# Kernel tuning notes

Measured on AMD Instinct MI355X. Metric: run time of the kernel, lower is better.

The kernel has to match this reference:

```python
import jax, jax.numpy as jnp
import numpy as np

N_NODES = 100000
N_EDGES = 800000
D = 128


def setup_inputs() -> dict:
    key = jax.random.key(0)
    ks = jax.random.split(key, 6)
    x = jax.random.normal(ks[0], (N_NODES, D), dtype=jnp.float32)
    src = jax.random.randint(ks[1], (N_EDGES,), 0, N_NODES, dtype=jnp.int64 if jax.config.jax_enable_x64 else jnp.int32)
    dst = jax.random.randint(ks[2], (N_EDGES,), 0, N_NODES, dtype=jnp.int64 if jax.config.jax_enable_x64 else jnp.int32)
    W_self = jax.random.normal(ks[3], (D, D), dtype=jnp.float32) / np.sqrt(D)
    W_neigh = jax.random.normal(ks[4], (D, D), dtype=jnp.float32) / np.sqrt(D)
    b = jax.random.normal(ks[5], (D,), dtype=jnp.float32) * 0.01
    return {"x": x, "src": src, "dst": dst, "W_self": W_self, "W_neigh": W_neigh, "b": b}


def reference(x, src, dst, W_self, W_neigh, b):
    # DGL SAGEConv('mean'): mean-aggregate source features over incoming edges.
    msgs = x[src]  # [E, D] gather (irregular)
    sums = jax.ops.segment_sum(msgs, dst, num_segments=N_NODES)  # [N, D]
    deg = jax.ops.segment_sum(jnp.ones((msgs.shape[0],), dtype=x.dtype), dst,
                              num_segments=N_NODES)
    # DGL clamps in-degree to at least 1 (zero-in-degree nodes get zero h_neigh).
    h_neigh = sums / jnp.maximum(deg, 1.0)[:, None]
    # rst = fc_self(h) + fc_neigh(h_neigh) + bias, then ReLU activation.
    out = x @ W_self + h_neigh @ W_neigh + b
    return jax.nn.relu(out)
```

## Files before the change

kernel.cpp:

```cpp
#include <hip/hip_runtime.h>
#include <stdint.h>

#define N_NODES 100000
#define N_EDGES 800000
#define D 128

typedef _Float16 f16x8 __attribute__((ext_vector_type(8)));
typedef float f32x4 __attribute__((ext_vector_type(4)));


__global__ void hist_rank(const int* __restrict__ dst, int* __restrict__ cnt,
                          int* __restrict__ rank) {
    int e = blockIdx.x * blockDim.x + threadIdx.x;
    if (e < N_EDGES) rank[e] = atomicAdd(&cnt[dst[e]], 1);
}

__global__ void scan_local(const int* __restrict__ cnt, int* __restrict__ offsets,
                           int* __restrict__ bs) {
    __shared__ int sdata[256];
    const int t = threadIdx.x;
    const int base = blockIdx.x * 1024 + t * 4;
    int v[4];
    int s = 0;
#pragma unroll
    for (int j = 0; j < 4; ++j) {
        int i = base + j;
        v[j] = (i < N_NODES) ? cnt[i] : 0;
        s += v[j];
    }
    sdata[t] = s;
    __syncthreads();
    int incl = s;
    for (int off = 1; off < 256; off <<= 1) {
        int add = (t >= off) ? sdata[t - off] : 0;
        __syncthreads();
        incl += add;
        sdata[t] = incl;
        __syncthreads();
    }
    int run = incl - s;
#pragma unroll
    for (int j = 0; j < 4; ++j) {
        int i = base + j;
        if (i < N_NODES) offsets[i] = run;
        run += v[j];
    }
    if (t == 255) bs[blockIdx.x] = incl;
}

__global__ void scan_block2(int* __restrict__ bs, int* __restrict__ offsets, int nblk) {
    int t = threadIdx.x;
    int v0 = (2 * t < nblk) ? bs[2 * t] : 0;
    int v1 = (2 * t + 1 < nblk) ? bs[2 * t + 1] : 0;
    int s = v0 + v1;
    int incl = s;
    for (int off = 1; off < 64; off <<= 1) {
        int n = __shfl_up(incl, off, 64);
        if (t >= off) incl += n;
    }
    int excl = incl - s;
    if (2 * t < nblk) bs[2 * t] = excl;
    if (2 * t + 1 < nblk) bs[2 * t + 1] = excl + v0;
    if (t == 63) offsets[N_NODES] = incl;
}

__global__ void scan_add(int* __restrict__ offsets, const int* __restrict__ bs) {
    const int t = threadIdx.x;
    const int base = blockIdx.x * 1024 + t * 4;
    const int add = bs[blockIdx.x];
#pragma unroll
    for (int j = 0; j < 4; ++j) {
        int i = base + j;
        if (i < N_NODES) offsets[i] += add;
    }
}

__global__ void scatter2(const int* __restrict__ src, const int* __restrict__ dst,
                         const int* __restrict__ offsets, const int* __restrict__ rank,
                         int* __restrict__ esrc) {
    int e = blockIdx.x * blockDim.x + threadIdx.x;
    if (e < N_EDGES) esrc[offsets[dst[e]] + rank[e]] = src[e];
}

__global__ __launch_bounds__(256) void gemm_reg(const float* __restrict__ x,
                                                const float* __restrict__ Ws,
                                                const float* __restrict__ Wn,
                                                const float* __restrict__ bias,
                                                float* __restrict__ pre,
                                                _Float16* __restrict__ y2) {
    const int half = blockIdx.x & 1;
    const int bid = blockIdx.x >> 1;
    const int nb = gridDim.x >> 1;
    const int tid = threadIdx.x;
    const int w = tid >> 6;
    const int lane = tid & 63;
    const int lr = lane & 15;
    const int lk = (lane >> 4) * 8;
    const int wc = w & 1;
    const int ws_ = w >> 1;

    const float* __restrict__ W = half ? Wn : Ws;

    f16x8 bfrag[4][4];
#pragma unroll
    for (int ks = 0; ks < 4; ++ks) {
#pragma unroll
        for (int fc = 0; fc < 4; ++fc) {
            const int col = wc * 64 + fc * 16 + lr;
            const int kb = ks * 32 + lk;
            f16x8 h;
#pragma unroll
            for (int j = 0; j < 8; ++j) h[j] = (_Float16)W[(long)(kb + j) * D + col];
            bfrag[ks][fc] = h;
        }
    }
    float bv[4];
    if (half == 0) {
#pragma unroll
        for (int fc = 0; fc < 4; ++fc) bv[fc] = bias[wc * 64 + fc * 16 + lr];
    }

    auto loadA = [&](f32x4* A, int s) {
        const float* __restrict__ xr = &x[(long)(s * 16 + lr) * D];
#pragma unroll
        for (int ks = 0; ks < 4; ++ks) {
            A[2 * ks] = *(const f32x4*)&xr[ks * 32 + lk];
            A[2 * ks + 1] = *(const f32x4*)&xr[ks * 32 + lk + 4];
        }
    };
    auto compStore = [&](const f32x4* A, int s) {
        f32x4 acc[4];
#pragma unroll
        for (int fc = 0; fc < 4; ++fc) acc[fc] = (f32x4){0.f, 0.f, 0.f, 0.f};
#pragma unroll
        for (int ks = 0; ks < 4; ++ks) {
            f16x8 af;
#pragma unroll
            for (int j = 0; j < 4; ++j) {
                af[j] = (_Float16)A[2 * ks][j];
                af[4 + j] = (_Float16)A[2 * ks + 1][j];
            }
#pragma unroll
            for (int fc = 0; fc < 4; ++fc)
                acc[fc] = __builtin_amdgcn_mfma_f32_16x16x32_f16(af, bfrag[ks][fc],
                                                                 acc[fc], 0, 0, 0);
        }
        const int rb = s * 16 + (lane >> 4) * 4;
        if (half == 0) {
#pragma unroll
            for (int fc = 0; fc < 4; ++fc) {
                const int col = wc * 64 + fc * 16 + lr;
#pragma unroll
                for (int i = 0; i < 4; ++i)
                    pre[(long)(rb + i) * D + col] = acc[fc][i] + bv[fc];
            }
        } else {
#pragma unroll
            for (int fc = 0; fc < 4; ++fc) {
                const int col = wc * 64 + fc * 16 + lr;
#pragma unroll
                for (int i = 0; i < 4; ++i)
                    y2[(long)(rb + i) * D + col] = (_Float16)acc[fc][i];
            }
        }
    };

    const int nstrip = N_NODES / 16;
    const int stride = nb * 2;
    int s = bid * 2 + ws_;
    int snext = s + stride;

    f32x4 A0[8], A1[8];
    loadA(A0, s);
    while (true) {
        bool hn = snext < nstrip;
        if (hn) loadA(A1, snext);
        compStore(A0, s);
        if (!hn) break;
        s = snext;
        snext += stride;
        hn = snext < nstrip;
        if (hn) loadA(A0, snext);
        compStore(A1, s);
        if (!hn) break;
        s = snext;
        snext += stride;
    }
}

__global__ __launch_bounds__(256) void agg_wave(const _Float16* __restrict__ y2,
                                                const int* __restrict__ offsets,
                                                const int* __restrict__ esrc,
                                                float* __restrict__ out) {
    const int n = blockIdx.x * 4 + (threadIdx.x >> 6);
    const int lane = threadIdx.x & 63;
    const int slot = lane >> 4;
    const int c8 = lane & 15;
    const int s = offsets[n];
    const int e = offsets[n + 1];
    float a[8] = {0.f, 0.f, 0.f, 0.f, 0.f, 0.f, 0.f, 0.f};
    for (int j = s + slot; j < e; j += 4) {
        int sn = esrc[j];
        f16x8 v = *(const f16x8*)&y2[(long)sn * D + c8 * 8];
#pragma unroll
        for (int i = 0; i < 8; ++i) a[i] += (float)v[i];
    }
#pragma unroll
    for (int i = 0; i < 8; ++i) {
        a[i] += __shfl_xor(a[i], 16, 64);
        a[i] += __shfl_xor(a[i], 32, 64);
    }
    if (slot == 0) {
        const int deg = e - s;
        const float inv = (deg > 0) ? 1.f / (float)deg : 0.f;
        float4 p0 = *(const float4*)&out[(long)n * D + c8 * 8];
        float4 p1 = *(const float4*)&out[(long)n * D + c8 * 8 + 4];
        float4 o0, o1;
        o0.x = fmaxf(p0.x + a[0] * inv, 0.f);
        o0.y = fmaxf(p0.y + a[1] * inv, 0.f);
        o0.z = fmaxf(p0.z + a[2] * inv, 0.f);
        o0.w = fmaxf(p0.w + a[3] * inv, 0.f);
        o1.x = fmaxf(p1.x + a[4] * inv, 0.f);
        o1.y = fmaxf(p1.y + a[5] * inv, 0.f);
        o1.z = fmaxf(p1.z + a[6] * inv, 0.f);
        o1.w = fmaxf(p1.w + a[7] * inv, 0.f);
        *(float4*)&out[(long)n * D + c8 * 8] = o0;
        *(float4*)&out[(long)n * D + c8 * 8 + 4] = o1;
    }
}


extern "C" void kernel_launch(void* const* d_in, const int* in_sizes, int n_in,
                              void* d_out, int out_size, void* d_ws, size_t ws_size,
                              hipStream_t stream) {
    const float* x  = (const float*)d_in[0];
    const int* src  = (const int*)d_in[1];
    const int* dst  = (const int*)d_in[2];
    const float* Ws = (const float*)d_in[3];
    const float* Wn = (const float*)d_in[4];
    const float* b  = (const float*)d_in[5];
    float* out = (float*)d_out;

    int* cnt     = (int*)d_ws;
    int* offsets = cnt + N_NODES;
    int* bs      = offsets + N_NODES + 1;
    int* rank    = bs + 128;
    int* esrc    = rank + N_EDGES;
    uintptr_t p = (uintptr_t)(esrc + N_EDGES);
    p = (p + 255) & ~(uintptr_t)255;
    _Float16* y2 = (_Float16*)p;

    const int nblk_scan = (N_NODES + 1023) / 1024;

    hipMemsetAsync(cnt, 0, N_NODES * sizeof(int), stream);
    hist_rank<<<(N_EDGES + 255) / 256, 256, 0, stream>>>(dst, cnt, rank);
    scan_local<<<nblk_scan, 256, 0, stream>>>(cnt, offsets, bs);
    scan_block2<<<1, 64, 0, stream>>>(bs, offsets, nblk_scan);
    scan_add<<<nblk_scan, 256, 0, stream>>>(offsets, bs);
    scatter2<<<(N_EDGES + 255) / 256, 256, 0, stream>>>(src, dst, offsets, rank, esrc);
    gemm_reg<<<1024, 256, 0, stream>>>(x, Ws, Wn, b, out, y2);
    agg_wave<<<N_NODES / 4, 256, 0, stream>>>(y2, offsets, esrc, out);
}
```

Measured before the change: 241.8 us.

## Fuse CSR build into one cooperative kernel with grid syncs

Replaces the memset plus five separate CSR-construction kernels (histogram, three scan stages, scatter) with a single cooperative kernel that uses grid-wide syncs between phases. This removes several kernel launch boundaries and their idle gaps. It also changes the gemm grid from 1024 to 1280 blocks. The risk is that each grid.sync costs time of its own, and the fixed 512-block grid may use the GPU less fully in the edge-parallel phases.

```diff
diff --git a/kernel.cpp b/kernel.cpp
--- a/kernel.cpp
+++ b/kernel.cpp
@@ -1,85 +1,102 @@
 #include <hip/hip_runtime.h>
+#include <hip/hip_cooperative_groups.h>
 #include <stdint.h>
+
+namespace cg = cooperative_groups;
 
 #define N_NODES 100000
 #define N_EDGES 800000
 #define D 128
+#define CSR_BLOCKS 512
+#define CSR_THREADS 256
 
 typedef _Float16 f16x8 __attribute__((ext_vector_type(8)));
 typedef float f32x4 __attribute__((ext_vector_type(4)));
 
-
-__global__ void hist_rank(const int* __restrict__ dst, int* __restrict__ cnt,
-                          int* __restrict__ rank) {
-    int e = blockIdx.x * blockDim.x + threadIdx.x;
-    if (e < N_EDGES) rank[e] = atomicAdd(&cnt[dst[e]], 1);
-}
-
-__global__ void scan_local(const int* __restrict__ cnt, int* __restrict__ offsets,
-                           int* __restrict__ bs) {
-    __shared__ int sdata[256];
+__global__ __launch_bounds__(CSR_THREADS) void csr_coop(const int* __restrict__ src,
+                                                        const int* __restrict__ dst,
+                                                        int* __restrict__ cnt,
+                                                        int* __restrict__ offsets,
+                                                        int* __restrict__ bs,
+                                                        int* __restrict__ rank,
+                                                        int* __restrict__ esrc) {
+    cg::grid_group grid = cg::this_grid();
+    __shared__ int sdata[CSR_THREADS];
     const int t = threadIdx.x;
-    const int base = blockIdx.x * 1024 + t * 4;
+    const int bid = blockIdx.x;
+    const int gtid = bid * CSR_THREADS + t;
+    const int gstride = CSR_BLOCKS * CSR_THREADS;
+
+    for (int i = gtid; i < N_NODES; i += gstride) cnt[i] = 0;
+    grid.sync();
+
+    for (int e = gtid; e < N_EDGES; e += gstride)
+        rank[e] = atomicAdd(&cnt[dst[e]], 1);
+    grid.sync();
+
+    const int nblk = (N_NODES + 1023) / 1024;
     int v[4];
-    int s = 0;
-#pragma unroll
-    for (int j = 0; j < 4; ++j) {
-        int i = base + j;
-        v[j] = (i < N_NODES) ? cnt[i] : 0;
-        s += v[j];
-    }
-    sdata[t] = s;
-    __syncthreads();
-    int incl = s;
-    for (int off = 1; off < 256; off <<= 1) {
-        int add = (t >= off) ? sdata[t - off] : 0;
+    int run_keep = 0;
+    if (bid < nblk) {
+        const int base = bid * 1024 + t * 4;
+        int s = 0;
+#pragma unroll
+        for (int j = 0; j < 4; ++j) {
+            int i = base + j;
+            v[j] = (i < N_NODES) ? cnt[i] : 0;
+            s += v[j];
+        }
+        sdata[t] = s;
         __syncthreads();
-        incl += add;
-        sdata[t] = incl;
-        __syncthreads();
-    }
-    int run = incl - s;
-#pragma unroll
-    for (int j = 0; j < 4; ++j) {
-        int i = base + j;
-        if (i < N_NODES) offsets[i] = run;
-        run += v[j];
-    }
-    if (t == 255) bs[blockIdx.x] = incl;
-}
-
-__global__ void scan_block2(int* __restrict__ bs, int* __restrict__ offsets, int nblk) {
-    int t = threadIdx.x;
-    int v0 = (2 * t < nblk) ? bs[2 * t] : 0;
-    int v1 = (2 * t + 1 < nblk) ? bs[2 * t + 1] : 0;
-    int s = v0 + v1;
-    int incl = s;
-    for (int off = 1; off < 64; off <<= 1) {
-        int n = __shfl_up(incl, off, 64);
-        if (t >= off) incl += n;
-    }
-    int excl = incl - s;
-    if (2 * t < nblk) bs[2 * t] = excl;
-    if (2 * t + 1 < nblk) bs[2 * t + 1] = excl + v0;
-    if (t == 63) offsets[N_NODES] = incl;
-}
-
-__global__ void scan_add(int* __restrict__ offsets, const int* __restrict__ bs) {
-    const int t = threadIdx.x;
-    const int base = blockIdx.x * 1024 + t * 4;
-    const int add = bs[blockIdx.x];
-#pragma unroll
-    for (int j = 0; j < 4; ++j) {
-        int i = base + j;
-        if (i < N_NODES) offsets[i] += add;
-    }
-}
-
-__global__ void scatter2(const int* __restrict__ src, const int* __restrict__ dst,
-                         const int* __restrict__ offsets, const int* __restrict__ rank,
-                         int* __restrict__ esrc) {
-    int e = blockIdx.x * blockDim.x + threadIdx.x;
-    if (e < N_EDGES) esrc[offsets[dst[e]] + rank[e]] = src[e];
+        int incl = s;
+        for (int off = 1; off < CSR_THREADS; off <<= 1) {
+            int add = (t >= off) ? sdata[t - off] : 0;
+            __syncthreads();
+            incl += add;
+            sdata[t] = incl;
+            __syncthreads();
+        }
+        int run = incl - s;
+        run_keep = run;
+#pragma unroll
+        for (int j = 0; j < 4; ++j) {
+            int i = base + j;
+            if (i < N_NODES) offsets[i] = run;
+            run += v[j];
+        }
+        if (t == CSR_THREADS - 1) bs[bid] = incl;
+    }
+    grid.sync();
+
+    if (bid == 0 && t < 64) {
+        int v0 = (2 * t < nblk) ? bs[2 * t] : 0;
+        int v1 = (2 * t + 1 < nblk) ? bs[2 * t + 1] : 0;
+        int s = v0 + v1;
+        int incl = s;
+        for (int off = 1; off < 64; off <<= 1) {
+            int n = __shfl_up(incl, off, 64);
+            if (t >= off) incl += n;
+        }
+        int excl = incl - s;
+        if (2 * t < nblk) bs[2 * t] = excl;
+        if (2 * t + 1 < nblk) bs[2 * t + 1] = excl + v0;
+        if (t == 63) offsets[N_NODES] = incl;
+    }
+    grid.sync();
+
+    if (bid < nblk) {
+        const int base = bid * 1024 + t * 4;
+        const int add = bs[bid];
+#pragma unroll
+        for (int j = 0; j < 4; ++j) {
+            int i = base + j;
+            if (i < N_NODES) offsets[i] += add;
+        }
+    }
+    grid.sync();
+
+    for (int e = gtid; e < N_EDGES; e += gstride)
+        esrc[offsets[dst[e]] + rank[e]] = src[e];
 }
 
 __global__ __launch_bounds__(256) void gemm_reg(const float* __restrict__ x,
@@ -250,14 +267,10 @@
     p = (p + 255) & ~(uintptr_t)255;
     _Float16* y2 = (_Float16*)p;
 
-    const int nblk_scan = (N_NODES + 1023) / 1024;
-
-    hipMemsetAsync(cnt, 0, N_NODES * sizeof(int), stream);
-    hist_rank<<<(N_EDGES + 255) / 256, 256, 0, stream>>>(dst, cnt, rank);
-    scan_local<<<nblk_scan, 256, 0, stream>>>(cnt, offsets, bs);
-    scan_block2<<<1, 64, 0, stream>>>(bs, offsets, nblk_scan);
-    scan_add<<<nblk_scan, 256, 0, stream>>>(offsets, bs);
-    scatter2<<<(N_EDGES + 255) / 256, 256, 0, stream>>>(src, dst, offsets, rank, esrc);
-    gemm_reg<<<1024, 256, 0, stream>>>(x, Ws, Wn, b, out, y2);
+    void* csr_args[] = {(void*)&src, (void*)&dst, (void*)&cnt, (void*)&offsets,
+                        (void*)&bs, (void*)&rank, (void*)&esrc};
+    hipLaunchCooperativeKernel((void*)csr_coop, dim3(CSR_BLOCKS), dim3(CSR_THREADS),
+                               csr_args, 0, stream);
+    gemm_reg<<<1280, 256, 0, stream>>>(x, Ws, Wn, b, out, y2);
     agg_wave<<<N_NODES / 4, 256, 0, stream>>>(y2, offsets, esrc, out);
 }
```

Result: slower. 515.3 us (+113.1%).

## Fold scan block offsets into consumers and vectorize histogram/scatter edge loads

Applied to the files above, without the earlier changes.

Removes the scan_add kernel by having the scatter and aggregation kernels add the per-block prefix (bs[n>>10]) on the fly, and derives the end offset of the last node from N_EDGES. The histogram and scatter kernels now process four edges per thread using int4 loads. The gemm grid is also raised from 1024 to 1280 blocks. This saves one launch and one pass over offsets, at the cost of an extra bs lookup in each consumer.

```diff
diff --git a/kernel.cpp b/kernel.cpp
--- a/kernel.cpp
+++ b/kernel.cpp
@@ -9,10 +9,18 @@
 typedef float f32x4 __attribute__((ext_vector_type(4)));
 
 
-__global__ void hist_rank(const int* __restrict__ dst, int* __restrict__ cnt,
-                          int* __restrict__ rank) {
-    int e = blockIdx.x * blockDim.x + threadIdx.x;
-    if (e < N_EDGES) rank[e] = atomicAdd(&cnt[dst[e]], 1);
+__global__ void hist_rank4(const int* __restrict__ dst, int* __restrict__ cnt,
+                           int* __restrict__ rank) {
+    int e4 = blockIdx.x * blockDim.x + threadIdx.x;
+    if (e4 < N_EDGES / 4) {
+        int4 d = ((const int4*)dst)[e4];
+        int4 r;
+        r.x = atomicAdd(&cnt[d.x], 1);
+        r.y = atomicAdd(&cnt[d.y], 1);
+        r.z = atomicAdd(&cnt[d.z], 1);
+        r.w = atomicAdd(&cnt[d.w], 1);
+        ((int4*)rank)[e4] = r;
+    }
 }
 
 __global__ void scan_local(const int* __restrict__ cnt, int* __restrict__ offsets,
@@ -48,7 +56,7 @@
     if (t == 255) bs[blockIdx.x] = incl;
 }
 
-__global__ void scan_block2(int* __restrict__ bs, int* __restrict__ offsets, int nblk) {
+__global__ void scan_block2(int* __restrict__ bs, int nblk) {
     int t = threadIdx.x;
     int v0 = (2 * t < nblk) ? bs[2 * t] : 0;
     int v1 = (2 * t + 1 < nblk) ? bs[2 * t + 1] : 0;
@@ -61,25 +69,21 @@
     int excl = incl - s;
     if (2 * t < nblk) bs[2 * t] = excl;
     if (2 * t + 1 < nblk) bs[2 * t + 1] = excl + v0;
-    if (t == 63) offsets[N_NODES] = incl;
-}
-
-__global__ void scan_add(int* __restrict__ offsets, const int* __restrict__ bs) {
-    const int t = threadIdx.x;
-    const int base = blockIdx.x * 1024 + t * 4;
-    const int add = bs[blockIdx.x];
-#pragma unroll
-    for (int j = 0; j < 4; ++j) {
-        int i = base + j;
-        if (i < N_NODES) offsets[i] += add;
-    }
-}
-
-__global__ void scatter2(const int* __restrict__ src, const int* __restrict__ dst,
-                         const int* __restrict__ offsets, const int* __restrict__ rank,
-                         int* __restrict__ esrc) {
-    int e = blockIdx.x * blockDim.x + threadIdx.x;
-    if (e < N_EDGES) esrc[offsets[dst[e]] + rank[e]] = src[e];
+}
+
+__global__ void scatter_f(const int* __restrict__ src, const int* __restrict__ dst,
+                          const int* __restrict__ offsets, const int* __restrict__ bs,
+                          const int* __restrict__ rank, int* __restrict__ esrc) {
+    int e4 = blockIdx.x * blockDim.x + threadIdx.x;
+    if (e4 < N_EDGES / 4) {
+        int4 d = ((const int4*)dst)[e4];
+        int4 sr = ((const int4*)src)[e4];
+        int4 r = ((const int4*)rank)[e4];
+        esrc[offsets[d.x] + bs[d.x >> 10] + r.x] = sr.x;
+        esrc[offsets[d.y] + bs[d.y >> 10] + r.y] = sr.y;
+        esrc[offsets[d.z] + bs[d.z >> 10] + r.z] = sr.z;
+        esrc[offsets[d.w] + bs[d.w >> 10] + r.w] = sr.w;
+    }
 }
 
 __global__ __launch_bounds__(256) void gemm_reg(const float* __restrict__ x,
@@ -188,16 +192,17 @@
     }
 }
 
-__global__ __launch_bounds__(256) void agg_wave(const _Float16* __restrict__ y2,
-                                                const int* __restrict__ offsets,
-                                                const int* __restrict__ esrc,
-                                                float* __restrict__ out) {
+__global__ __launch_bounds__(256) void agg_wave2(const _Float16* __restrict__ y2,
+                                                 const int* __restrict__ offsets,
+                                                 const int* __restrict__ bs,
+                                                 const int* __restrict__ esrc,
+                                                 float* __restrict__ out) {
     const int n = blockIdx.x * 4 + (threadIdx.x >> 6);
     const int lane = threadIdx.x & 63;
     const int slot = lane >> 4;
     const int c8 = lane & 15;
-    const int s = offsets[n];
-    const int e = offsets[n + 1];
+    const int s = offsets[n] + bs[n >> 10];
+    const int e = (n == N_NODES - 1) ? N_EDGES : offsets[n + 1] + bs[(n + 1) >> 10];
     float a[8] = {0.f, 0.f, 0.f, 0.f, 0.f, 0.f, 0.f, 0.f};
     for (int j = s + slot; j < e; j += 4) {
         int sn = esrc[j];
@@ -253,11 +258,11 @@
     const int nblk_scan = (N_NODES + 1023) / 1024;
 
     hipMemsetAsync(cnt, 0, N_NODES * sizeof(int), stream);
-    hist_rank<<<(N_EDGES + 255) / 256, 256, 0, stream>>>(dst, cnt, rank);
+    hist_rank4<<<(N_EDGES / 4 + 255) / 256, 256, 0, stream>>>(dst, cnt, rank);
     scan_local<<<nblk_scan, 256, 0, stream>>>(cnt, offsets, bs);
-    scan_block2<<<1, 64, 0, stream>>>(bs, offsets, nblk_scan);
-    scan_add<<<nblk_scan, 256, 0, stream>>>(offsets, bs);
-    scatter2<<<(N_EDGES + 255) / 256, 256, 0, stream>>>(src, dst, offsets, rank, esrc);
-    gemm_reg<<<1024, 256, 0, stream>>>(x, Ws, Wn, b, out, y2);
-    agg_wave<<<N_NODES / 4, 256, 0, stream>>>(y2, offsets, esrc, out);
-}
+    scan_block2<<<1, 64, 0, stream>>>(bs, nblk_scan);
+    scatter_f<<<(N_EDGES / 4 + 255) / 256, 256, 0, stream>>>(src, dst, offsets, bs,
+                                                             rank, esrc);
+    gemm_reg<<<1280, 256, 0, stream>>>(x, Ws, Wn, b, out, y2);
+    agg_wave2<<<N_NODES / 4, 256, 0, stream>>>(y2, offsets, bs, esrc, out);
+}
```

Result: no change. 246.1 us (+1.7%).
